# Performance work log

Hardware: AMD Instinct MI355X
Metric: run time of the kernel (lower is better)

## Reference

```python
import jax, jax.numpy as jnp
import numpy as np

B, T, D, H = 4, 2048, 2048, 16
DH = D // H

def setup_inputs() -> dict:
    key = jax.random.key(0)
    ks = jax.random.split(key, 9)
    s = 1.0 / np.sqrt(D)
    return {
        "x": jax.random.normal(ks[0], (B, T, D), dtype=jnp.float32),
        "Wq": jax.random.uniform(ks[1], (D, D), jnp.float32, -s, s),
        "bq": jax.random.uniform(ks[2], (D,), jnp.float32, -s, s),
        "Wk": jax.random.uniform(ks[3], (D, D), jnp.float32, -s, s),
        "bk": jax.random.uniform(ks[4], (D,), jnp.float32, -s, s),
        "Wv": jax.random.uniform(ks[5], (D, D), jnp.float32, -s, s),
        "bv": jax.random.uniform(ks[6], (D,), jnp.float32, -s, s),
        "Wo": jax.random.uniform(ks[7], (D, D), jnp.float32, -s, s),
        "bo": jax.random.uniform(ks[8], (D,), jnp.float32, -s, s),
    }

def reference(x, Wq, bq, Wk, bk, Wv, bv, Wo, bo):
    # projections: [B,T,D] -> [B,H,T,DH]
    def split_heads(y):
        return y.reshape(B, T, H, DH).transpose(0, 2, 1, 3)
    q = split_heads(x @ Wq + bq)
    k = split_heads(x @ Wk + bk)
    v = split_heads(x @ Wv + bv)
    scale = DH ** -0.5
    scores = jnp.einsum('bhtd,bhsd->bhts', q, k) * scale  # [B,H,T,T]
    causal = jnp.tril(jnp.ones((T, T), dtype=bool))
    scores = jnp.where(causal[None, None], scores, -jnp.inf)
    weights = jax.nn.softmax(scores, axis=-1)
    out = jnp.einsum('bhts,bhsd->bhtd', weights, v)  # [B,H,T,DH]
    out = out.transpose(0, 2, 1, 3).reshape(B, T, D)
    return out @ Wo + bo
```

## Files before the change

### kernel.cpp

```cpp
#include <hip/hip_runtime.h>
#include <hip/hip_bf16.h>

#define B_  4
#define T_  2048
#define D_  2048
#define H_  16
#define DH_ 128
#define KG  2048

typedef __attribute__((ext_vector_type(4))) float f32x4;
typedef __attribute__((ext_vector_type(8))) short short8;
typedef __attribute__((ext_vector_type(4))) _Float16 half4;

__device__ __forceinline__ ushort f2bf(float f) {
    unsigned int u = __builtin_bit_cast(unsigned int, f);
    u += 0x7fffu + ((u >> 16) & 1u);
    return (ushort)(u >> 16);
}
__device__ __forceinline__ ushort f2h(float f) {
    return (ushort)(__builtin_bit_cast(unsigned int, __builtin_amdgcn_cvt_pkrtz(f, f)) & 0xffffu);
}

__device__ __forceinline__ void glds16(const void* g, void* l) {
    __builtin_amdgcn_global_load_lds(
        (const __attribute__((address_space(1))) unsigned int*)g,
        (__attribute__((address_space(3))) unsigned int*)l, 16, 0, 0);
}

__global__ void cast_f32_bf16(const float* __restrict__ x, ushort* __restrict__ xb, int n) {
    int i = (blockIdx.x * 256 + threadIdx.x) * 4;
    if (i < n) {
        float4 v = *(const float4*)(x + i);
        ushort4 o;
        o.x = f2bf(v.x); o.y = f2bf(v.y); o.z = f2bf(v.z); o.w = f2bf(v.w);
        *(ushort4*)(xb + i) = o;
    }
}

__global__ void transpose_cast(const float* __restrict__ W, ushort* __restrict__ Wt) {
    __shared__ float tile[32][33];
    int tx = threadIdx.x, ty = threadIdx.y;
    int n0 = blockIdx.x * 32, k0 = blockIdx.y * 32;
#pragma unroll
    for (int i = 0; i < 4; i++)
        tile[ty + i * 8][tx] = W[(size_t)(k0 + ty + i * 8) * D_ + n0 + tx];
    __syncthreads();
#pragma unroll
    for (int i = 0; i < 4; i++)
        Wt[(size_t)(n0 + ty + i * 8) * D_ + k0 + tx] = f2bf(tile[tx][ty + i * 8]);
}


#define LDS_A(d, qm, AF)                                                                   \
  { _Pragma("unroll") for (int mt = 0; mt < 4; ++mt) {                                     \
      AF[mt][0] = __builtin_bit_cast(short8,                                               \
          *(const uint4*)(smem + aAddr0 + (((d)*2 + (qm)) << 14) + mt*2048));              \
      AF[mt][1] = __builtin_bit_cast(short8,                                               \
          *(const uint4*)(smem + aAddr1 + (((d)*2 + (qm)) << 14) + mt*2048));              \
    } }

#define LDS_B(d, qn, BF)                                                                   \
  { _Pragma("unroll") for (int nt = 0; nt < 2; ++nt) {                                     \
      BF[nt][0] = __builtin_bit_cast(short8,                                               \
          *(const uint4*)(smem + bAddr0 + (((d)*2 + (qn)) << 14) + nt*2048));              \
      BF[nt][1] = __builtin_bit_cast(short8,                                               \
          *(const uint4*)(smem + bAddr1 + (((d)*2 + (qn)) << 14) + nt*2048));              \
    } }

#define STAGE_A(d, qm, kt)                                                                 \
  { const ushort* s_ = aSrc + (size_t)(qm) * (64 * KG) + (size_t)(kt) * 64;                \
    char* l_ = ldsT + (((d)*2 + (qm)) << 14);                                              \
    glds16(s_, l_);                                                                        \
    glds16(s_ + (size_t)128 * KG, l_ + 8192); }

#define STAGE_B(d, qn, kt)                                                                 \
  { const ushort* s_ = bSrc + (size_t)(qn) * (32 * KG) + (size_t)(kt) * 64;                \
    char* l_ = ldsT + 65536 + (((d)*2 + (qn)) << 14);                                      \
    glds16(s_, l_);                                                                        \
    glds16(s_ + (size_t)128 * KG, l_ + 8192); }

#define MFMA16(QM, QN, AF, BF)                                                             \
  __builtin_amdgcn_s_setprio(1);                                                           \
  _Pragma("unroll") for (int mt = 0; mt < 4; ++mt)                                         \
    _Pragma("unroll") for (int nt = 0; nt < 2; ++nt)                                       \
      _Pragma("unroll") for (int kk = 0; kk < 2; ++kk)                                     \
        acc[(QM)*4 + mt][(QN)*2 + nt] = __builtin_amdgcn_mfma_f32_16x16x32_bf16(           \
            AF[mt][kk], BF[nt][kk], acc[(QM)*4 + mt][(QN)*2 + nt], 0, 0, 0);               \
  __builtin_amdgcn_s_setprio(0);

#define BAR1_LGKM  __builtin_amdgcn_s_barrier();                                           \
                   asm volatile("s_waitcnt lgkmcnt(0)" ::: "memory");
#define BAR2       __builtin_amdgcn_s_barrier();
#define VM4        asm volatile("s_waitcnt vmcnt(4)" ::: "memory");
#define VM2        asm volatile("s_waitcnt vmcnt(2)" ::: "memory");
#define VM0        asm volatile("s_waitcnt vmcnt(0)" ::: "memory");

#define GEMM256_PRE                                                                        \
    const int lane = tid & 63, w = tid >> 6;                                               \
    const int l15 = lane & 15, quad = lane >> 4;                                           \
    const int wm = w & 1, wn = w >> 1;                                                     \
    const int irow = tid >> 3;                                                             \
    const int chl  = (tid & 7) ^ (irow & 7);                                               \
    const ushort* aSrc = Ap + (size_t)(row0 + irow) * KG + chl * 8;                        \
    const ushort* bSrc = Bp + (size_t)(col0 + ((irow >> 5) << 6) + (irow & 31)) * KG + chl * 8; \
    char* ldsT = smem + tid * 16;                                                          \
    const int sw0 = (quad ^ (l15 & 7)) << 4;                                               \
    const int sw1 = ((4 + quad) ^ (l15 & 7)) << 4;                                         \
    const int aRow = (wm * 64 + l15) * 128;                                                \
    const int bRow = (wn * 32 + l15) * 128;                                                \
    const int aAddr0 = aRow + sw0, aAddr1 = aRow + sw1;                                    \
    const int bAddr0 = 65536 + bRow + sw0, bAddr1 = 65536 + bRow + sw1;

#define GEMM256_MAIN_LOOP                                                                  \
    f32x4 acc[8][4] = {};                                                                  \
    short8 aF[4][2], bF[2][2];                                                             \
    STAGE_A(0, 0, 0); STAGE_B(0, 0, 0); STAGE_A(0, 1, 0); STAGE_B(0, 1, 0);                \
    STAGE_A(1, 0, 1);                                                                      \
    VM2; __builtin_amdgcn_s_barrier();                                                     \
    _Pragma("unroll 1")                                                                    \
    for (int j = 0; j < 16; ++j) {                                                         \
        const int t1 = 2*j + 1;                                                            \
        const int t2 = (2*j + 2 < 32) ? 2*j + 2 : 31;                                      \
        const int t3 = (2*j + 3 < 32) ? 2*j + 3 : 31;                                      \
         LDS_A(0, 0, aF); LDS_B(0, 0, bF);                                         \
                 STAGE_A(1, 1, t1); STAGE_B(1, 0, t1);                                     \
                 BAR1_LGKM; MFMA16(0, 0, aF, bF); BAR2;                                    \
         LDS_B(0, 1, bF); STAGE_B(1, 1, t1);                                       \
                 BAR1_LGKM; MFMA16(0, 1, aF, bF); BAR2;                                    \
         LDS_A(0, 1, aF); STAGE_A(0, 0, t2);                                       \
                 BAR1_LGKM; MFMA16(1, 1, aF, bF); BAR2;                                    \
         LDS_B(0, 0, bF); STAGE_A(0, 1, t2);                                       \
                 BAR1_LGKM; MFMA16(1, 0, aF, bF); VM4; BAR2;                               \
         LDS_A(1, 0, aF); LDS_B(1, 0, bF); STAGE_B(0, 0, t2);                      \
                 BAR1_LGKM; MFMA16(0, 0, aF, bF); BAR2;                                    \
         LDS_B(1, 1, bF); STAGE_B(0, 1, t2);                                       \
                 BAR1_LGKM; MFMA16(0, 1, aF, bF); BAR2;                                    \
         LDS_A(1, 1, aF); STAGE_A(1, 0, t3);                                       \
                 BAR1_LGKM; MFMA16(1, 1, aF, bF); BAR2;                                    \
         LDS_B(1, 0, bF);                                                          \
                 BAR1_LGKM; MFMA16(1, 0, aF, bF); VM2; BAR2;                               \
    }                                                                                      \
    VM0; __builtin_amdgcn_s_barrier();

__global__ __launch_bounds__(512, 2) void gemm_qkv256(
    const ushort* __restrict__ A,
    const ushort* __restrict__ Wq, const ushort* __restrict__ Wk, const ushort* __restrict__ Wv,
    const float* __restrict__ bq, const float* __restrict__ bk, const float* __restrict__ bv,
    ushort* __restrict__ Qb, ushort* __restrict__ Kb, ushort* __restrict__ Vtb,
    float qscale)
{
    extern __shared__ char smem[];
    const int tid = threadIdx.x;

    int id = blockIdx.y * 24 + blockIdx.x;
    id = (id & 7) * 96 + (id >> 3);
    const int bx = id % 24, by = id / 24;

    const int sel  = bx >> 3;
    const int row0 = by * 256, col0 = (bx & 7) * 256;
    const ushort* Ap = A;
    const ushort* Bp = (sel == 0) ? Wq : (sel == 1) ? Wk : Wv;
    const float* bias = (sel == 0) ? bq : (sel == 1) ? bk : bv;
    const float oscale = (sel == 0) ? qscale : 1.0f;

    GEMM256_PRE
    GEMM256_MAIN_LOOP

    if (sel < 2) {
        ushort* Cout = sel ? Kb : Qb;
#pragma unroll
        for (int ntg = 0; ntg < 4; ++ntg) {
            int col = col0 + wn * 64 + ntg * 16 + l15;
            float bb = bias[col];
#pragma unroll
            for (int mtg = 0; mtg < 8; ++mtg) {
                int rowb = row0 + wm * 128 + mtg * 16 + quad * 4;
#pragma unroll
                for (int r = 0; r < 4; ++r)
                    Cout[(size_t)(rowb + r) * D_ + col] = f2bf((acc[mtg][ntg][r] + bb) * oscale);
            }
        }
    } else {
        const int b = row0 >> 11, t0 = (row0 & (T_ - 1)) + wm * 128;
        const int h = (col0 + wn * 64) >> 7;
        ushort* eT = (ushort*)smem + w * (32 * 136);
#pragma unroll 1
        for (int rnd = 0; rnd < 2; ++rnd) {
#pragma unroll
            for (int ni = 0; ni < 2; ++ni) {
                int ntg = rnd * 2 + ni;
                int col = col0 + wn * 64 + ntg * 16 + l15;
                float bb = bias[col];
#pragma unroll
                for (int mtg = 0; mtg < 8; ++mtg)
#pragma unroll
                    for (int r = 0; r < 4; ++r)
                        eT[(ni * 16 + l15) * 136 + mtg * 16 + quad * 4 + r] = f2h(acc[mtg][ntg][r] + bb);
            }
            int dhbase = ((wn & 1) ? 64 : 0) + rnd * 32;
#pragma unroll
            for (int it = 0; it < 8; ++it) {
                int chunk = it * 64 + lane;
                int d2 = chunk >> 4, c = chunk & 15;
                uint4 v = *(const uint4*)(eT + d2 * 136 + c * 8);
                *(uint4*)(Vtb + (size_t)((b * H_ + h) * DH_ + dhbase + d2) * T_ + t0 + c * 8) = v;
            }
        }
    }
}

__global__ __launch_bounds__(512, 2) void gemm_o256(
    const ushort* __restrict__ A, const ushort* __restrict__ Bt,
    const float* __restrict__ bias, float* __restrict__ Cout)
{
    extern __shared__ char smem[];
    const int tid = threadIdx.x;

    int id = blockIdx.y * 8 + blockIdx.x;
    id = (id & 7) * 32 + (id >> 3);
    const int bx = id % 8, by = id / 8;

    const int row0 = by * 256, col0 = bx * 256;
    const ushort* Ap = A;
    const ushort* Bp = Bt;

    GEMM256_PRE
    GEMM256_MAIN_LOOP

#pragma unroll
    for (int ntg = 0; ntg < 4; ++ntg) {
        int col = col0 + wn * 64 + ntg * 16 + l15;
        float bb = bias[col];
#pragma unroll
        for (int mtg = 0; mtg < 8; ++mtg) {
            int rowb = row0 + wm * 128 + mtg * 16 + quad * 4;
#pragma unroll
            for (int r = 0; r < 4; ++r)
                Cout[(size_t)(rowb + r) * D_ + col] = acc[mtg][ntg][r] + bb;
        }
    }
}

__global__ __launch_bounds__(256, 5) void attn_kernel(
    const ushort* __restrict__ Q, const ushort* __restrict__ K,
    const ushort* __restrict__ Vt, ushort* __restrict__ O)
{
    __shared__ __align__(16) char smem[32768];
    uint4*  kS = (uint4*)smem;
    ushort* vS = (ushort*)(smem + 16384);

    const int tid = threadIdx.x;
    const int bid = blockIdx.x;
    const int slot = bid >> 3;
    const int g = (bid & 7) + 8 * (slot >> 4);
    const int qx = slot & 15;
    const int b = g >> 4, h = g & 15;

    const int lane = tid & 63, w = tid >> 6, l15 = lane & 15, quad = lane >> 4;

    const int krow = tid >> 4;
    const int kchunk = (tid & 15) ^ (krow & 7);
    const ushort* kg = K + ((size_t)(b * T_) + krow) * D_ + h * DH_ + kchunk * 8;

    const int vrow = tid >> 3, vc = tid & 7;
    const ushort* vg = Vt + ((size_t)((b * H_ + h) * DH_) + vrow) * T_ + vc * 8;
    const int vs0 = ((2 * vc    ) ^ (vrow & 15)) * 4;
    const int vs1 = ((2 * vc + 1) ^ (vrow & 15)) * 4;

    const int qts[2] = { qx, 31 - qx };

    for (int e = 0; e < 2; ++e) {
        const int qt = qts[e], q0 = qt * 64;
        const int qbase = q0 + w * 16;

        short8 aq[4];
        {
            const ushort* qp = Q + ((size_t)(b * T_) + qbase + l15) * D_ + h * DH_ + quad * 8;
#pragma unroll
            for (int ks = 0; ks < 4; ++ks)
                aq[ks] = __builtin_bit_cast(short8, *(const uint4*)(qp + ks * 32));
        }

        f32x4 accO[8] = {};
        float mrow = -INFINITY, lrow = 0.f;

        auto tile = [&](int s0, int stMax, bool diag) {
            __syncthreads();
            const ushort* kp = kg + (size_t)s0 * D_;
#pragma unroll
            for (int j = 0; j < 4; ++j) glds16(kp + (size_t)j * 16 * D_, kS + j * 256 + tid);
            const ushort* vp = vg + s0;
            uint4 vv[4];
#pragma unroll
            for (int j = 0; j < 4; ++j) vv[j] = *(const uint4*)(vp + (size_t)j * 32 * T_);
#pragma unroll
            for (int j = 0; j < 4; ++j) {
                ushort* dst = vS + (j * 32 + vrow) * 64;
                *(uint2*)(dst + vs0) = make_uint2(vv[j].x, vv[j].y);
                *(uint2*)(dst + vs1) = make_uint2(vv[j].z, vv[j].w);
            }
            __syncthreads();

            f32x4 sT[4] = {};
#pragma unroll
            for (int ks = 0; ks < 4; ++ks)
#pragma unroll
                for (int st = 0; st < 4; ++st)
                    if (st < stMax) {
                        int row = st * 16 + l15;
                        short8 ak = __builtin_bit_cast(short8, kS[row * 16 + ((ks * 4 + quad) ^ (row & 7))]);
                        sT[st] = __builtin_amdgcn_mfma_f32_16x16x32_bf16(ak, aq[ks], sT[st], 0, 0, 0);
                    }

            if (diag) {
                const int q = qbase + l15;
                const int st = stMax - 1;
#pragma unroll
                for (int r = 0; r < 4; ++r)
                    if (s0 + st * 16 + quad * 4 + r > q) sT[st][r] = -INFINITY;
            }

            float rmax = -INFINITY;
#pragma unroll
            for (int st = 0; st < 4; ++st)
                if (st < stMax)
#pragma unroll
                    for (int r = 0; r < 4; ++r) rmax = fmaxf(rmax, sT[st][r]);
            rmax = fmaxf(rmax, __shfl_xor(rmax, 16));
            rmax = fmaxf(rmax, __shfl_xor(rmax, 32));
            float mnew  = fmaxf(mrow, rmax);
            float alpha = __builtin_amdgcn_exp2f(mrow - mnew);
            mrow = mnew;

            float psum = 0.f;
            half4 pb[4];
#pragma unroll
            for (int st = 0; st < 4; ++st)
                if (st < stMax) {
                    float p0 = __builtin_amdgcn_exp2f(sT[st][0] - mnew);
                    float p1 = __builtin_amdgcn_exp2f(sT[st][1] - mnew);
                    float p2 = __builtin_amdgcn_exp2f(sT[st][2] - mnew);
                    float p3 = __builtin_amdgcn_exp2f(sT[st][3] - mnew);
                    psum += (p0 + p1) + (p2 + p3);
                    uint2 u;
                    u.x = __builtin_bit_cast(unsigned int, __builtin_amdgcn_cvt_pkrtz(p0, p1));
                    u.y = __builtin_bit_cast(unsigned int, __builtin_amdgcn_cvt_pkrtz(p2, p3));
                    pb[st] = __builtin_bit_cast(half4, u);
                }
            psum += __shfl_xor(psum, 16);
            psum += __shfl_xor(psum, 32);
            lrow = lrow * alpha + psum;
#pragma unroll
            for (int nt = 0; nt < 8; ++nt)
#pragma unroll
                for (int r = 0; r < 4; ++r) accO[nt][r] *= alpha;

#pragma unroll
            for (int st = 0; st < 4; ++st)
                if (st < stMax) {
#pragma unroll
                    for (int nt = 0; nt < 8; ++nt) {
                        int dh = nt * 16 + l15;
                        half4 vf = *(const half4*)(vS + dh * 64 + (((st * 4 + quad) ^ l15) * 4));
                        accO[nt] = __builtin_amdgcn_mfma_f32_16x16x16f16(vf, pb[st], accO[nt], 0, 0, 0);
                    }
                }
        };

        for (int it = 0; it < qt; ++it) tile(it * 64, 4, false);
        tile(qt * 64, w + 1, true);

        __syncthreads();
        ushort* eT = (ushort*)smem + w * 2176;
        float inv = 1.0f / lrow;
#pragma unroll
        for (int nt = 0; nt < 8; ++nt) {
            int dh = nt * 16 + quad * 4;
#pragma unroll
            for (int r = 0; r < 4; ++r)
                eT[l15 * 136 + dh + r] = f2bf(accO[nt][r] * inv);
        }
        for (int idx = lane; idx < 256; idx += 64) {
            int row = idx >> 4, c = idx & 15;
            uint4 v = *(const uint4*)(eT + row * 136 + c * 8);
            *(uint4*)(O + ((size_t)(b * T_) + q0 + w * 16 + row) * D_ + h * DH_ + c * 8) = v;
        }
    }
}

extern "C" void kernel_launch(void* const* d_in, const int* in_sizes, int n_in,
                              void* d_out, int out_size, void* d_ws, size_t ws_size,
                              hipStream_t stream) {
    const float* x  = (const float*)d_in[0];
    const float* Wq = (const float*)d_in[1];
    const float* bq = (const float*)d_in[2];
    const float* Wk = (const float*)d_in[3];
    const float* bk = (const float*)d_in[4];
    const float* Wv = (const float*)d_in[5];
    const float* bv = (const float*)d_in[6];
    const float* Wo = (const float*)d_in[7];
    const float* bo = (const float*)d_in[8];

    char* ws = (char*)d_ws;
    const size_t MB = 1u << 20;
    ushort* xb  = (ushort*)(ws);
    ushort* Wqt = (ushort*)(ws + 32 * MB);
    ushort* Wkt = (ushort*)(ws + 40 * MB);
    ushort* Wvt = (ushort*)(ws + 48 * MB);
    ushort* Wot = (ushort*)(ws + 56 * MB);
    ushort* Qb  = (ushort*)(ws + 64 * MB);
    ushort* Kb  = (ushort*)(ws + 96 * MB);
    ushort* Vtb = (ushort*)(ws + 128 * MB);
    ushort* Ob  = (ushort*)(ws + 160 * MB);

    const int M = B_ * T_;
    const float qscale = (float)(0.08838834764831845 * 1.4426950408889634);

    static bool attr_done = false;
    if (!attr_done) {
        (void)hipFuncSetAttribute((const void*)gemm_qkv256,
                                  hipFuncAttributeMaxDynamicSharedMemorySize, 131072);
        (void)hipFuncSetAttribute((const void*)gemm_o256,
                                  hipFuncAttributeMaxDynamicSharedMemorySize, 131072);
        attr_done = true;
    }

    cast_f32_bf16<<<(M * D_) / 1024, 256, 0, stream>>>(x, xb, M * D_);
    dim3 tb(32, 8), tg(D_ / 32, D_ / 32);
    transpose_cast<<<tg, tb, 0, stream>>>(Wq, Wqt);
    transpose_cast<<<tg, tb, 0, stream>>>(Wk, Wkt);
    transpose_cast<<<tg, tb, 0, stream>>>(Wv, Wvt);
    transpose_cast<<<tg, tb, 0, stream>>>(Wo, Wot);

    gemm_qkv256<<<dim3(24, M / 256), 512, 131072, stream>>>(
        xb, Wqt, Wkt, Wvt, bq, bk, bv, Qb, Kb, Vtb, qscale);

    attn_kernel<<<dim3(1024), 256, 0, stream>>>(Qb, Kb, Vtb, Ob);

    gemm_o256<<<dim3(D_ / 256, M / 256), 512, 131072, stream>>>(
        Ob, Wot, bo, (float*)d_out);
}
```

Measured before the change: 683.6 us.

## Deepen GEMM LDS prefetch pipeline, remap block order, reorder epilogue stores

Reworks the shared GEMM main loop so more global-to-LDS stages are in flight. The prologue issues seven stage loads and waits at vmcnt(6), and each sub-step now waits vmcnt(6) plus barriers with sched_barrier fences, replacing the lgkmcnt-based sync. The QKV grid mapping is changed to a contiguous per-XCD column grouping, the O-projection swizzle is removed, and the epilogues hoist the bias loads and iterate columns innermost. The goal is to hide global load latency behind the MFMAs and improve L2 locality. The risk is an LDS read/write race if the reordered stage slots and wait counts do not line up.

```diff
diff --git a/kernel.cpp b/kernel.cpp
--- a/kernel.cpp
+++ b/kernel.cpp
@@ -88,12 +88,10 @@
             AF[mt][kk], BF[nt][kk], acc[(QM)*4 + mt][(QN)*2 + nt], 0, 0, 0);               \
   __builtin_amdgcn_s_setprio(0);
 
-#define BAR1_LGKM  __builtin_amdgcn_s_barrier();                                           \
-                   asm volatile("s_waitcnt lgkmcnt(0)" ::: "memory");
-#define BAR2       __builtin_amdgcn_s_barrier();
-#define VM4        asm volatile("s_waitcnt vmcnt(4)" ::: "memory");
-#define VM2        asm volatile("s_waitcnt vmcnt(2)" ::: "memory");
+#define VM6        asm volatile("s_waitcnt vmcnt(6)" ::: "memory");
 #define VM0        asm volatile("s_waitcnt vmcnt(0)" ::: "memory");
+#define BARR       __builtin_amdgcn_s_barrier();
+#define SCHEDB     __builtin_amdgcn_sched_barrier(0);
 
 #define GEMM256_PRE                                                                        \
     const int lane = tid & 63, w = tid >> 6;                                               \
@@ -114,33 +112,33 @@
 #define GEMM256_MAIN_LOOP                                                                  \
     f32x4 acc[8][4] = {};                                                                  \
     short8 aF[4][2], bF[2][2];                                                             \
-    STAGE_A(0, 0, 0); STAGE_B(0, 0, 0); STAGE_A(0, 1, 0); STAGE_B(0, 1, 0);                \
-    STAGE_A(1, 0, 1);                                                                      \
-    VM2; __builtin_amdgcn_s_barrier();                                                     \
+        \
+    STAGE_A(0, 0, 0); STAGE_B(0, 1, 0); STAGE_A(0, 1, 0); STAGE_B(0, 0, 0);                \
+    STAGE_A(1, 0, 1); STAGE_B(1, 1, 1); STAGE_A(1, 1, 1);                                  \
+    VM6; BARR; SCHEDB;                                                                     \
     _Pragma("unroll 1")                                                                    \
     for (int j = 0; j < 16; ++j) {                                                         \
         const int t1 = 2*j + 1;                                                            \
         const int t2 = (2*j + 2 < 32) ? 2*j + 2 : 31;                                      \
         const int t3 = (2*j + 3 < 32) ? 2*j + 3 : 31;                                      \
-         LDS_A(0, 0, aF); LDS_B(0, 0, bF);                                         \
-                 STAGE_A(1, 1, t1); STAGE_B(1, 0, t1);                                     \
-                 BAR1_LGKM; MFMA16(0, 0, aF, bF); BAR2;                                    \
-         LDS_B(0, 1, bF); STAGE_B(1, 1, t1);                                       \
-                 BAR1_LGKM; MFMA16(0, 1, aF, bF); BAR2;                                    \
-         LDS_A(0, 1, aF); STAGE_A(0, 0, t2);                                       \
-                 BAR1_LGKM; MFMA16(1, 1, aF, bF); BAR2;                                    \
+         LDS_A(0, 0, aF); LDS_B(0, 0, bF); STAGE_B(1, 0, t1);                      \
+                 VM6; BARR; MFMA16(0, 0, aF, bF); BARR; SCHEDB;                            \
+         LDS_B(0, 1, bF); STAGE_A(0, 0, t2);                                       \
+                 VM6; BARR; MFMA16(0, 1, aF, bF); BARR; SCHEDB;                            \
+         LDS_A(0, 1, aF); STAGE_B(0, 1, t2);                                       \
+                 VM6; BARR; MFMA16(1, 1, aF, bF); BARR; SCHEDB;                            \
          LDS_B(0, 0, bF); STAGE_A(0, 1, t2);                                       \
-                 BAR1_LGKM; MFMA16(1, 0, aF, bF); VM4; BAR2;                               \
+                 VM6; BARR; MFMA16(1, 0, aF, bF); BARR; SCHEDB;                            \
          LDS_A(1, 0, aF); LDS_B(1, 0, bF); STAGE_B(0, 0, t2);                      \
-                 BAR1_LGKM; MFMA16(0, 0, aF, bF); BAR2;                                    \
-         LDS_B(1, 1, bF); STAGE_B(0, 1, t2);                                       \
-                 BAR1_LGKM; MFMA16(0, 1, aF, bF); BAR2;                                    \
-         LDS_A(1, 1, aF); STAGE_A(1, 0, t3);                                       \
-                 BAR1_LGKM; MFMA16(1, 1, aF, bF); BAR2;                                    \
-         LDS_B(1, 0, bF);                                                          \
-                 BAR1_LGKM; MFMA16(1, 0, aF, bF); VM2; BAR2;                               \
+                 VM6; BARR; MFMA16(0, 0, aF, bF); BARR; SCHEDB;                            \
+         LDS_B(1, 1, bF); STAGE_A(1, 0, t3);                                       \
+                 VM6; BARR; MFMA16(0, 1, aF, bF); BARR; SCHEDB;                            \
+         LDS_A(1, 1, aF); STAGE_B(1, 1, t3);                                       \
+                 VM6; BARR; MFMA16(1, 1, aF, bF); BARR; SCHEDB;                            \
+         LDS_B(1, 0, bF); STAGE_A(1, 1, t3);                                       \
+                 VM6; BARR; MFMA16(1, 0, aF, bF); BARR; SCHEDB;                            \
     }                                                                                      \
-    VM0; __builtin_amdgcn_s_barrier();
+    VM0; BARR;
 
 __global__ __launch_bounds__(512, 2) void gemm_qkv256(
     const ushort* __restrict__ A,
@@ -152,9 +150,10 @@
     extern __shared__ char smem[];
     const int tid = threadIdx.x;
 
-    int id = blockIdx.y * 24 + blockIdx.x;
-    id = (id & 7) * 96 + (id >> 3);
-    const int bx = id % 24, by = id / 24;
+    const int lid = blockIdx.y * 24 + blockIdx.x;
+    const int xcd = lid & 7, jj = lid >> 3;
+    const int bx  = 3 * xcd + jj % 3;
+    const int by  = jj / 3;
 
     const int sel  = bx >> 3;
     const int row0 = by * 256, col0 = (bx & 7) * 256;
@@ -168,17 +167,19 @@
 
     if (sel < 2) {
         ushort* Cout = sel ? Kb : Qb;
-#pragma unroll
-        for (int ntg = 0; ntg < 4; ++ntg) {
-            int col = col0 + wn * 64 + ntg * 16 + l15;
-            float bb = bias[col];
-#pragma unroll
-            for (int mtg = 0; mtg < 8; ++mtg) {
-                int rowb = row0 + wm * 128 + mtg * 16 + quad * 4;
-#pragma unroll
-                for (int r = 0; r < 4; ++r)
-                    Cout[(size_t)(rowb + r) * D_ + col] = f2bf((acc[mtg][ntg][r] + bb) * oscale);
-            }
+        float bb[4];
+#pragma unroll
+        for (int ntg = 0; ntg < 4; ++ntg) bb[ntg] = bias[col0 + wn * 64 + ntg * 16 + l15];
+#pragma unroll
+        for (int mtg = 0; mtg < 8; ++mtg) {
+            int rowb = row0 + wm * 128 + mtg * 16 + quad * 4;
+#pragma unroll
+            for (int r = 0; r < 4; ++r)
+#pragma unroll
+                for (int ntg = 0; ntg < 4; ++ntg) {
+                    int col = col0 + wn * 64 + ntg * 16 + l15;
+                    Cout[(size_t)(rowb + r) * D_ + col] = f2bf((acc[mtg][ntg][r] + bb[ntg]) * oscale);
+                }
         }
     } else {
         const int b = row0 >> 11, t0 = (row0 & (T_ - 1)) + wm * 128;
@@ -216,10 +217,7 @@
     extern __shared__ char smem[];
     const int tid = threadIdx.x;
 
-    int id = blockIdx.y * 8 + blockIdx.x;
-    id = (id & 7) * 32 + (id >> 3);
-    const int bx = id % 8, by = id / 8;
-
+    const int bx = blockIdx.x, by = blockIdx.y;
     const int row0 = by * 256, col0 = bx * 256;
     const ushort* Ap = A;
     const ushort* Bp = Bt;
@@ -227,17 +225,19 @@
     GEMM256_PRE
     GEMM256_MAIN_LOOP
 
-#pragma unroll
-    for (int ntg = 0; ntg < 4; ++ntg) {
-        int col = col0 + wn * 64 + ntg * 16 + l15;
-        float bb = bias[col];
-#pragma unroll
-        for (int mtg = 0; mtg < 8; ++mtg) {
-            int rowb = row0 + wm * 128 + mtg * 16 + quad * 4;
-#pragma unroll
-            for (int r = 0; r < 4; ++r)
-                Cout[(size_t)(rowb + r) * D_ + col] = acc[mtg][ntg][r] + bb;
-        }
+    float bb[4];
+#pragma unroll
+    for (int ntg = 0; ntg < 4; ++ntg) bb[ntg] = bias[col0 + wn * 64 + ntg * 16 + l15];
+#pragma unroll
+    for (int mtg = 0; mtg < 8; ++mtg) {
+        int rowb = row0 + wm * 128 + mtg * 16 + quad * 4;
+#pragma unroll
+        for (int r = 0; r < 4; ++r)
+#pragma unroll
+            for (int ntg = 0; ntg < 4; ++ntg) {
+                int col = col0 + wn * 64 + ntg * 16 + l15;
+                Cout[(size_t)(rowb + r) * D_ + col] = acc[mtg][ntg][r] + bb[ntg];
+            }
     }
 }
 
```

Measured after the change: 677.2 us. No clear change (-0.9%).
